# Performance work log

Hardware: AMD Instinct MI355X
Metric: run time of the kernel (lower is better)

Reference implementation:

```python
import jax, jax.numpy as jnp
import numpy as np

N, F = 8192, 64
SLOPE = 3.0


def _mlp(h, params):
    # params: list of (W[in,out], b[out]); Tanh after EVERY linear (incl. last)
    for W, b in params:
        h = jnp.tanh(h @ W + b)
    return h


def setup_inputs() -> dict:
    key = jax.random.key(0)
    ks = jax.random.split(key, 16)
    x = jax.random.normal(ks[0], (N, F, 2), dtype=jnp.float32)
    def lin(k, fi, fo):
        k1, k2 = jax.random.split(k)
        s = 1.0 / np.sqrt(fi)
        W = jax.random.uniform(k1, (fi, fo), jnp.float32, -s, s)
        b = jax.random.uniform(k2, (fo,), jnp.float32, -s, s)
        return W, b
    w_in1, b_in1 = lin(ks[1], 2, 4)
    w_in2, b_in2 = lin(ks[2], 4, 4)
    w_in3, b_in3 = lin(ks[3], 4, 1)
    w_a1, b_a1 = lin(ks[4], 1, 2)
    w_a2, b_a2 = lin(ks[5], 2, 1)
    w_b1, b_b1 = lin(ks[6], 1, 2)
    w_b2, b_b2 = lin(ks[7], 2, 1)
    return dict(x=x,
                w_in1=w_in1, b_in1=b_in1, w_in2=w_in2, b_in2=b_in2,
                w_in3=w_in3, b_in3=b_in3,
                w_a1=w_a1, b_a1=b_a1, w_a2=w_a2, b_a2=b_a2,
                w_b1=w_b1, b_b1=b_b1, w_b2=w_b2, b_b2=b_b2)


def reference(x, w_in1, b_in1, w_in2, b_in2, w_in3, b_in3,
              w_a1, b_a1, w_a2, b_a2, w_b1, b_b1, w_b2, b_b2):
    n, f = x.shape[0], x.shape[1]
    # per-coordinate-pair encode: [N*F,2] -> [N*F,1] -> [N,F]
    h = _mlp(x.reshape(-1, 2), [(w_in1, b_in1), (w_in2, b_in2), (w_in3, b_in3)])
    xe = h.reshape(n, f)
    # dense self-attention aggregation, softmax over dim 0 (columns normalized)
    attn = jax.nn.softmax(xe @ xe.T, axis=0)  # [N,N]
    xe = attn @ xe                            # [N,F]
    # pairwise squared euclidean distances E[i,j] = ||x_i - x_j||^2
    sq = jnp.sum(xe * xe, axis=1)             # [N]
    E = sq[:, None] + sq[None, :] - 2.0 * (xe @ xe.T)
    m = jnp.mean(E).reshape(1)                # [1]
    alpha = jnp.exp(SLOPE * _mlp(m, [(w_a1, b_a1), (w_a2, b_a2)]))
    beta = jnp.exp(-SLOPE * _mlp(m, [(w_b1, b_b1), (w_b2, b_b2)]))
    return xe, alpha, beta
```

## Files before the change

### kernel.cpp

```cpp
#include <hip/hip_runtime.h>
#include <cstdint>

typedef __bf16 bf16x8 __attribute__((ext_vector_type(8)));
typedef __bf16 bf16x4 __attribute__((ext_vector_type(4)));
typedef float  f32x4  __attribute__((ext_vector_type(4)));

#define N_PTS 8192
#define FDIM  64
#define NF    (N_PTS * FDIM)

__device__ __forceinline__ float ftanh(float x) {
    float e = __expf(2.f * x);
    return 1.f - 2.f / (e + 1.f);
}

__global__ __launch_bounds__(256) void k_encode(
    const float* __restrict__ x,
    const float* __restrict__ w1, const float* __restrict__ b1,
    const float* __restrict__ w2, const float* __restrict__ b2,
    const float* __restrict__ w3, const float* __restrict__ b3,
    __bf16* __restrict__ xe)
{
    int idx = blockIdx.x * 256 + threadIdx.x;
    float2 p = ((const float2*)x)[idx];
    float h1[4], h2[4];
#pragma unroll
    for (int o = 0; o < 4; o++)
        h1[o] = ftanh(p.x * w1[o] + p.y * w1[4 + o] + b1[o]);
#pragma unroll
    for (int o = 0; o < 4; o++) {
        float s = b2[o];
#pragma unroll
        for (int i = 0; i < 4; i++) s += h1[i] * w2[i * 4 + o];
        h2[o] = ftanh(s);
    }
    float s3 = b3[0];
#pragma unroll
    for (int i = 0; i < 4; i++) s3 += h2[i] * w3[i];
    xe[idx] = (__bf16)ftanh(s3);
}

__global__ __launch_bounds__(256) void k_pass1(
    const __bf16* __restrict__ xe, float* __restrict__ D)
{
    __shared__ __bf16 sJ[64 * 64];
    __shared__ __bf16 sI[64 * 64];
    const int tid = threadIdx.x;
    const int j0 = blockIdx.x * 64;
    const int ibase = blockIdx.y * 2048;

#pragma unroll
    for (int k = 0; k < 2; k++) {
        int seg = tid + k * 256; int r = seg >> 3, c8 = seg & 7;
        *(uint4*)(sJ + r * 64 + c8 * 8) = *(const uint4*)(xe + (j0 + r) * 64 + c8 * 8);
    }
    __syncthreads();

    const int wave = tid >> 6, lane = tid & 63, c = lane & 15, q = lane >> 4;
    bf16x8 a0 = *(const bf16x8*)(sJ + (16 * wave + c) * 64 + q * 8);
    bf16x8 a1 = *(const bf16x8*)(sJ + (16 * wave + c) * 64 + 32 + q * 8);

    f32x4 esum = {0.f, 0.f, 0.f, 0.f};
    for (int ic = 0; ic < 32; ic++) {
        __syncthreads();
#pragma unroll
        for (int k = 0; k < 2; k++) {
            int seg = tid + k * 256; int r = seg >> 3, c8 = seg & 7;
            *(uint4*)(sI + r * 64 + c8 * 8) =
                *(const uint4*)(xe + (ibase + ic * 64 + r) * 64 + c8 * 8);
        }
        __syncthreads();
#pragma unroll
        for (int it = 0; it < 4; it++) {
            bf16x8 b0 = *(const bf16x8*)(sI + (16 * it + c) * 64 + q * 8);
            bf16x8 b1 = *(const bf16x8*)(sI + (16 * it + c) * 64 + 32 + q * 8);
            f32x4 s = {0.f, 0.f, 0.f, 0.f};
            s = __builtin_amdgcn_mfma_f32_16x16x32_bf16(a0, b0, s, 0, 0, 0);
            s = __builtin_amdgcn_mfma_f32_16x16x32_bf16(a1, b1, s, 0, 0, 0);
            esum.x += __expf(s.x); esum.y += __expf(s.y);
            esum.z += __expf(s.z); esum.w += __expf(s.w);
        }
    }
#pragma unroll
    for (int m = 1; m < 16; m <<= 1) {
        esum.x += __shfl_xor(esum.x, m); esum.y += __shfl_xor(esum.y, m);
        esum.z += __shfl_xor(esum.z, m); esum.w += __shfl_xor(esum.w, m);
    }
    if (c == 0) {
        atomicAdd(&D[j0 + 16 * wave + 4 * q + 0], esum.x);
        atomicAdd(&D[j0 + 16 * wave + 4 * q + 1], esum.y);
        atomicAdd(&D[j0 + 16 * wave + 4 * q + 2], esum.z);
        atomicAdd(&D[j0 + 16 * wave + 4 * q + 3], esum.w);
    }
}

__global__ __launch_bounds__(256) void k_build_u(
    const __bf16* __restrict__ xe, const float* __restrict__ D,
    __bf16* __restrict__ uT)
{
    __shared__ __bf16 T[64 * 72];
    const int tid = threadIdx.x;
    const int j0 = blockIdx.x * 64;
    const int r = tid >> 2, cg = tid & 3;
    float invd = 1.0f / D[j0 + r];
    bf16x8 v0 = *(const bf16x8*)(xe + (j0 + r) * 64 + cg * 16);
    bf16x8 v1 = *(const bf16x8*)(xe + (j0 + r) * 64 + cg * 16 + 8);
#pragma unroll
    for (int e = 0; e < 8; e++) {
        T[(cg * 16 + e) * 72 + r]     = (__bf16)((float)v0[e] * invd);
        T[(cg * 16 + 8 + e) * 72 + r] = (__bf16)((float)v1[e] * invd);
    }
    __syncthreads();
    uint4 w0 = *(uint4*)((char*)T + r * 144 + cg * 32);
    uint4 w1 = *(uint4*)((char*)T + r * 144 + cg * 32 + 16);
    *(uint4*)(uT + r * 8192 + j0 + cg * 16)     = w0;
    *(uint4*)(uT + r * 8192 + j0 + cg * 16 + 8) = w1;
}

__global__ __launch_bounds__(256) void k_pass2(
    const __bf16* __restrict__ xe, const __bf16* __restrict__ uT,
    float* __restrict__ out)
{
    __shared__ __bf16 sI[128 * 64];
    __shared__ __bf16 sJ[64 * 64];
    __shared__ __bf16 sU[64 * 64];
    __shared__ __bf16 sP[128 * 72];
    const int tid = threadIdx.x;
    const int ibase = blockIdx.x * 128;
    const int jbase = blockIdx.y * 1024;

#pragma unroll
    for (int k = 0; k < 4; k++) {
        int seg = tid + k * 256; int r = seg >> 3, c8 = seg & 7;
        *(uint4*)(sI + r * 64 + c8 * 8) = *(const uint4*)(xe + (ibase + r) * 64 + c8 * 8);
    }
    __syncthreads();

    const int wave = tid >> 6, lane = tid & 63, c = lane & 15, q = lane >> 4;
    bf16x8 bst[2][2];
#pragma unroll
    for (int isub = 0; isub < 2; isub++)
#pragma unroll
        for (int kc = 0; kc < 2; kc++)
            bst[isub][kc] = *(const bf16x8*)(sI + (32 * wave + 16 * isub + c) * 64 + kc * 32 + q * 8);

    f32x4 o[2][4];
#pragma unroll
    for (int a = 0; a < 2; a++)
#pragma unroll
        for (int b = 0; b < 4; b++) o[a][b] = (f32x4){0.f, 0.f, 0.f, 0.f};

    for (int jc = 0; jc < 16; jc++) {
        const int j0 = jbase + jc * 64;
        __syncthreads();
#pragma unroll
        for (int k = 0; k < 2; k++) {
            int seg = tid + k * 256; int r = seg >> 3, c8 = seg & 7;
            *(uint4*)(sJ + r * 64 + c8 * 8) = *(const uint4*)(xe + (j0 + r) * 64 + c8 * 8);
            *(uint4*)(sU + r * 64 + c8 * 8) = *(const uint4*)(uT + r * 8192 + j0 + c8 * 8);
        }
        __syncthreads();

#pragma unroll
        for (int jt = 0; jt < 4; jt++) {
            bf16x8 a0 = *(const bf16x8*)(sJ + (16 * jt + c) * 64 + q * 8);
            bf16x8 a1 = *(const bf16x8*)(sJ + (16 * jt + c) * 64 + 32 + q * 8);
#pragma unroll
            for (int isub = 0; isub < 2; isub++) {
                f32x4 s = {0.f, 0.f, 0.f, 0.f};
                s = __builtin_amdgcn_mfma_f32_16x16x32_bf16(a0, bst[isub][0], s, 0, 0, 0);
                s = __builtin_amdgcn_mfma_f32_16x16x32_bf16(a1, bst[isub][1], s, 0, 0, 0);
                bf16x4 pv;
                pv[0] = (__bf16)__expf(s[0]); pv[1] = (__bf16)__expf(s[1]);
                pv[2] = (__bf16)__expf(s[2]); pv[3] = (__bf16)__expf(s[3]);
                *(bf16x4*)(sP + (32 * wave + 16 * isub + c) * 72 + 16 * jt + 4 * q) = pv;
            }
        }
#pragma unroll
        for (int kc = 0; kc < 2; kc++) {
            bf16x8 ap0 = *(const bf16x8*)(sP + (32 * wave + c) * 72 + kc * 32 + q * 8);
            bf16x8 ap1 = *(const bf16x8*)(sP + (32 * wave + 16 + c) * 72 + kc * 32 + q * 8);
#pragma unroll
            for (int ft = 0; ft < 4; ft++) {
                bf16x8 bu = *(const bf16x8*)(sU + (16 * ft + c) * 64 + kc * 32 + q * 8);
                o[0][ft] = __builtin_amdgcn_mfma_f32_16x16x32_bf16(ap0, bu, o[0][ft], 0, 0, 0);
                o[1][ft] = __builtin_amdgcn_mfma_f32_16x16x32_bf16(ap1, bu, o[1][ft], 0, 0, 0);
            }
        }
    }
#pragma unroll
    for (int isub = 0; isub < 2; isub++)
#pragma unroll
        for (int ft = 0; ft < 4; ft++)
#pragma unroll
            for (int r = 0; r < 4; r++)
                atomicAdd(&out[(ibase + 32 * wave + 16 * isub + 4 * q + r) * 64 + 16 * ft + c],
                          o[isub][ft][r]);
}

__global__ __launch_bounds__(256) void k_combine(
    const float* __restrict__ out, float* __restrict__ colp,
    float* __restrict__ sqp)
{
    const int tid = threadIdx.x;
    const int base = blockIdx.x * 256 + tid;
    float col = 0.f, sq = 0.f;
#pragma unroll
    for (int k = 0; k < 8; k++) {
        float o = out[base + k * 65536];
        col += o; sq += o * o;
    }
    __shared__ float sv[256];
    __shared__ float sw[4];
    sv[tid] = col;
#pragma unroll
    for (int m = 32; m; m >>= 1) sq += __shfl_xor(sq, m);
    if ((tid & 63) == 0) sw[tid >> 6] = sq;
    __syncthreads();
    if (tid < 64) {
        float t = sv[tid] + sv[tid + 64] + sv[tid + 128] + sv[tid + 192];
        colp[blockIdx.x * 64 + tid] = t;
    }
    if (tid == 0) sqp[blockIdx.x] = sw[0] + sw[1] + sw[2] + sw[3];
}

__global__ void k_final(
    const float* __restrict__ colp, const float* __restrict__ sqp,
    const float* __restrict__ wa1, const float* __restrict__ ba1,
    const float* __restrict__ wa2, const float* __restrict__ ba2,
    const float* __restrict__ wb1, const float* __restrict__ bb1,
    const float* __restrict__ wb2, const float* __restrict__ bb2,
    float* __restrict__ out_tail)
{
    const int f = threadIdx.x;
    float colsum = 0.f;
    for (int b = 0; b < 256; b++) colsum += colp[b * 64 + f];
    float ss = colsum * colsum;
#pragma unroll
    for (int m = 32; m; m >>= 1) ss += __shfl_xor(ss, m);
    float sq = 0.f;
#pragma unroll
    for (int k = 0; k < 4; k++) sq += sqp[f + 64 * k];
#pragma unroll
    for (int m = 32; m; m >>= 1) sq += __shfl_xor(sq, m);
    if (f == 0) {
        const float invN = 1.f / 8192.f;
        float m = 2.f * invN * sq - 2.f * invN * invN * ss;
        float h0 = tanhf(m * wa1[0] + ba1[0]);
        float h1 = tanhf(m * wa1[1] + ba1[1]);
        float a  = tanhf(h0 * wa2[0] + h1 * wa2[1] + ba2[0]);
        float g0 = tanhf(m * wb1[0] + bb1[0]);
        float g1 = tanhf(m * wb1[1] + bb1[1]);
        float b  = tanhf(g0 * wb2[0] + g1 * wb2[1] + bb2[0]);
        out_tail[0] = __expf(3.f * a);
        out_tail[1] = __expf(-3.f * b);
    }
}

extern "C" void kernel_launch(void* const* d_in, const int* in_sizes, int n_in,
                              void* d_out, int out_size, void* d_ws, size_t ws_size,
                              hipStream_t stream)
{
    const float* x     = (const float*)d_in[0];
    const float* w_in1 = (const float*)d_in[1];
    const float* b_in1 = (const float*)d_in[2];
    const float* w_in2 = (const float*)d_in[3];
    const float* b_in2 = (const float*)d_in[4];
    const float* w_in3 = (const float*)d_in[5];
    const float* b_in3 = (const float*)d_in[6];
    const float* w_a1  = (const float*)d_in[7];
    const float* b_a1  = (const float*)d_in[8];
    const float* w_a2  = (const float*)d_in[9];
    const float* b_a2  = (const float*)d_in[10];
    const float* w_b1  = (const float*)d_in[11];
    const float* b_b1  = (const float*)d_in[12];
    const float* w_b2  = (const float*)d_in[13];
    const float* b_b2  = (const float*)d_in[14];

    float* out = (float*)d_out;
    char*  ws  = (char*)d_ws;
    __bf16* xe = (__bf16*)ws;
    __bf16* uT = (__bf16*)(ws + (1 << 20));
    float*  D  = (float*)(ws + (2 << 20));
    float*  colp = (float*)(ws + (2 << 20) + 32768);
    float*  sqp  = (float*)(ws + (2 << 20) + 32768 + 65536);

    hipMemsetAsync(D, 0, N_PTS * sizeof(float), stream);
    hipMemsetAsync(out, 0, (size_t)out_size * sizeof(float), stream);

    k_encode<<<NF / 256, 256, 0, stream>>>(x, w_in1, b_in1, w_in2, b_in2, w_in3, b_in3, xe);
    k_pass1<<<dim3(128, 4), 256, 0, stream>>>(xe, D);
    k_build_u<<<128, 256, 0, stream>>>(xe, D, uT);
    k_pass2<<<dim3(64, 8), 256, 0, stream>>>(xe, uT, out);
    k_combine<<<NF / 256 / 8, 256, 0, stream>>>(out, colp, sqp);
    k_final<<<1, 64, 0, stream>>>(colp, sqp, w_a1, b_a1, w_a2, b_a2,
                                  w_b1, b_b1, w_b2, b_b2, out + NF);
}
```

Measured before the change: 171.6 us.

## Replace atomics with partial buffers and double grid parallelism in both passes

Pass1 now keeps the J-tile fragments in registers, streams 128-row I tiles, and writes per-block column partial sums to a buffer instead of issuing atomics. Pass2 doubles the grid along j and writes per-split partial outputs, and k_combine reduces the 16 partials, which removes both the output atomics and the memsets. LDS rows are padded to 72 elements to reduce bank conflicts. The cost is extra workspace traffic: 16 full output-sized partial buffers are written and then read back in the combine step.

```diff
diff --git a/kernel.cpp b/kernel.cpp
--- a/kernel.cpp
+++ b/kernel.cpp
@@ -41,68 +41,68 @@
 }
 
 __global__ __launch_bounds__(256) void k_pass1(
-    const __bf16* __restrict__ xe, float* __restrict__ D)
-{
-    __shared__ __bf16 sJ[64 * 64];
-    __shared__ __bf16 sI[64 * 64];
+    const __bf16* __restrict__ xe, float* __restrict__ Dp)
+{
+    __shared__ __bf16 sI[128 * 72];
     const int tid = threadIdx.x;
     const int j0 = blockIdx.x * 64;
-    const int ibase = blockIdx.y * 2048;
-
-#pragma unroll
-    for (int k = 0; k < 2; k++) {
-        int seg = tid + k * 256; int r = seg >> 3, c8 = seg & 7;
-        *(uint4*)(sJ + r * 64 + c8 * 8) = *(const uint4*)(xe + (j0 + r) * 64 + c8 * 8);
-    }
-    __syncthreads();
-
+    const int ibase = blockIdx.y * 1024;
     const int wave = tid >> 6, lane = tid & 63, c = lane & 15, q = lane >> 4;
-    bf16x8 a0 = *(const bf16x8*)(sJ + (16 * wave + c) * 64 + q * 8);
-    bf16x8 a1 = *(const bf16x8*)(sJ + (16 * wave + c) * 64 + 32 + q * 8);
-
-    f32x4 esum = {0.f, 0.f, 0.f, 0.f};
-    for (int ic = 0; ic < 32; ic++) {
-        __syncthreads();
-#pragma unroll
-        for (int k = 0; k < 2; k++) {
+
+    bf16x8 Bf[4][2];
+#pragma unroll
+    for (int jt = 0; jt < 4; jt++)
+#pragma unroll
+        for (int kc = 0; kc < 2; kc++)
+            Bf[jt][kc] = *(const bf16x8*)(xe + (j0 + 16 * jt + c) * 64 + kc * 32 + q * 8);
+
+    float es[4] = {0.f, 0.f, 0.f, 0.f};
+    for (int ic = 0; ic < 8; ic++) {
+        __syncthreads();
+#pragma unroll
+        for (int k = 0; k < 4; k++) {
             int seg = tid + k * 256; int r = seg >> 3, c8 = seg & 7;
-            *(uint4*)(sI + r * 64 + c8 * 8) =
-                *(const uint4*)(xe + (ibase + ic * 64 + r) * 64 + c8 * 8);
-        }
-        __syncthreads();
-#pragma unroll
-        for (int it = 0; it < 4; it++) {
-            bf16x8 b0 = *(const bf16x8*)(sI + (16 * it + c) * 64 + q * 8);
-            bf16x8 b1 = *(const bf16x8*)(sI + (16 * it + c) * 64 + 32 + q * 8);
-            f32x4 s = {0.f, 0.f, 0.f, 0.f};
-            s = __builtin_amdgcn_mfma_f32_16x16x32_bf16(a0, b0, s, 0, 0, 0);
-            s = __builtin_amdgcn_mfma_f32_16x16x32_bf16(a1, b1, s, 0, 0, 0);
-            esum.x += __expf(s.x); esum.y += __expf(s.y);
-            esum.z += __expf(s.z); esum.w += __expf(s.w);
-        }
-    }
-#pragma unroll
-    for (int m = 1; m < 16; m <<= 1) {
-        esum.x += __shfl_xor(esum.x, m); esum.y += __shfl_xor(esum.y, m);
-        esum.z += __shfl_xor(esum.z, m); esum.w += __shfl_xor(esum.w, m);
-    }
-    if (c == 0) {
-        atomicAdd(&D[j0 + 16 * wave + 4 * q + 0], esum.x);
-        atomicAdd(&D[j0 + 16 * wave + 4 * q + 1], esum.y);
-        atomicAdd(&D[j0 + 16 * wave + 4 * q + 2], esum.z);
-        atomicAdd(&D[j0 + 16 * wave + 4 * q + 3], esum.w);
+            *(uint4*)(sI + r * 72 + c8 * 8) =
+                *(const uint4*)(xe + (ibase + ic * 128 + r) * 64 + c8 * 8);
+        }
+        __syncthreads();
+#pragma unroll
+        for (int g = 0; g < 2; g++) {
+            bf16x8 a0 = *(const bf16x8*)(sI + (32 * wave + 16 * g + c) * 72 + q * 8);
+            bf16x8 a1 = *(const bf16x8*)(sI + (32 * wave + 16 * g + c) * 72 + 32 + q * 8);
+#pragma unroll
+            for (int jt = 0; jt < 4; jt++) {
+                f32x4 s = {0.f, 0.f, 0.f, 0.f};
+                s = __builtin_amdgcn_mfma_f32_16x16x32_bf16(a0, Bf[jt][0], s, 0, 0, 0);
+                s = __builtin_amdgcn_mfma_f32_16x16x32_bf16(a1, Bf[jt][1], s, 0, 0, 0);
+                es[jt] += __expf(s.x) + __expf(s.y) + __expf(s.z) + __expf(s.w);
+            }
+        }
+    }
+#pragma unroll
+    for (int jt = 0; jt < 4; jt++) {
+        es[jt] += __shfl_xor(es[jt], 16);
+        es[jt] += __shfl_xor(es[jt], 32);
+    }
+    if (q == 0) {
+        float* d = Dp + (blockIdx.y * 4 + wave) * N_PTS + j0;
+#pragma unroll
+        for (int jt = 0; jt < 4; jt++) d[16 * jt + c] = es[jt];
     }
 }
 
 __global__ __launch_bounds__(256) void k_build_u(
-    const __bf16* __restrict__ xe, const float* __restrict__ D,
+    const __bf16* __restrict__ xe, const float* __restrict__ Dp,
     __bf16* __restrict__ uT)
 {
     __shared__ __bf16 T[64 * 72];
     const int tid = threadIdx.x;
     const int j0 = blockIdx.x * 64;
     const int r = tid >> 2, cg = tid & 3;
-    float invd = 1.0f / D[j0 + r];
+    float dsum = 0.f;
+#pragma unroll
+    for (int s = 0; s < 32; s++) dsum += Dp[s * N_PTS + j0 + r];
+    float invd = 1.0f / dsum;
     bf16x8 v0 = *(const bf16x8*)(xe + (j0 + r) * 64 + cg * 16);
     bf16x8 v1 = *(const bf16x8*)(xe + (j0 + r) * 64 + cg * 16 + 8);
 #pragma unroll
@@ -119,30 +119,22 @@
 
 __global__ __launch_bounds__(256) void k_pass2(
     const __bf16* __restrict__ xe, const __bf16* __restrict__ uT,
-    float* __restrict__ out)
-{
-    __shared__ __bf16 sI[128 * 64];
-    __shared__ __bf16 sJ[64 * 64];
-    __shared__ __bf16 sU[64 * 64];
+    float* __restrict__ outp)
+{
+    __shared__ __bf16 sJ[64 * 72];
+    __shared__ __bf16 sU[64 * 72];
     __shared__ __bf16 sP[128 * 72];
     const int tid = threadIdx.x;
     const int ibase = blockIdx.x * 128;
-    const int jbase = blockIdx.y * 1024;
-
-#pragma unroll
-    for (int k = 0; k < 4; k++) {
-        int seg = tid + k * 256; int r = seg >> 3, c8 = seg & 7;
-        *(uint4*)(sI + r * 64 + c8 * 8) = *(const uint4*)(xe + (ibase + r) * 64 + c8 * 8);
-    }
-    __syncthreads();
-
+    const int jbase = blockIdx.y * 512;
     const int wave = tid >> 6, lane = tid & 63, c = lane & 15, q = lane >> 4;
+
     bf16x8 bst[2][2];
 #pragma unroll
     for (int isub = 0; isub < 2; isub++)
 #pragma unroll
         for (int kc = 0; kc < 2; kc++)
-            bst[isub][kc] = *(const bf16x8*)(sI + (32 * wave + 16 * isub + c) * 64 + kc * 32 + q * 8);
+            bst[isub][kc] = *(const bf16x8*)(xe + (ibase + 32 * wave + 16 * isub + c) * 64 + kc * 32 + q * 8);
 
     f32x4 o[2][4];
 #pragma unroll
@@ -150,21 +142,21 @@
 #pragma unroll
         for (int b = 0; b < 4; b++) o[a][b] = (f32x4){0.f, 0.f, 0.f, 0.f};
 
-    for (int jc = 0; jc < 16; jc++) {
+    for (int jc = 0; jc < 8; jc++) {
         const int j0 = jbase + jc * 64;
         __syncthreads();
 #pragma unroll
         for (int k = 0; k < 2; k++) {
             int seg = tid + k * 256; int r = seg >> 3, c8 = seg & 7;
-            *(uint4*)(sJ + r * 64 + c8 * 8) = *(const uint4*)(xe + (j0 + r) * 64 + c8 * 8);
-            *(uint4*)(sU + r * 64 + c8 * 8) = *(const uint4*)(uT + r * 8192 + j0 + c8 * 8);
+            *(uint4*)(sJ + r * 72 + c8 * 8) = *(const uint4*)(xe + (j0 + r) * 64 + c8 * 8);
+            *(uint4*)(sU + r * 72 + c8 * 8) = *(const uint4*)(uT + r * 8192 + j0 + c8 * 8);
         }
         __syncthreads();
 
 #pragma unroll
         for (int jt = 0; jt < 4; jt++) {
-            bf16x8 a0 = *(const bf16x8*)(sJ + (16 * jt + c) * 64 + q * 8);
-            bf16x8 a1 = *(const bf16x8*)(sJ + (16 * jt + c) * 64 + 32 + q * 8);
+            bf16x8 a0 = *(const bf16x8*)(sJ + (16 * jt + c) * 72 + q * 8);
+            bf16x8 a1 = *(const bf16x8*)(sJ + (16 * jt + c) * 72 + 32 + q * 8);
 #pragma unroll
             for (int isub = 0; isub < 2; isub++) {
                 f32x4 s = {0.f, 0.f, 0.f, 0.f};
@@ -182,33 +174,38 @@
             bf16x8 ap1 = *(const bf16x8*)(sP + (32 * wave + 16 + c) * 72 + kc * 32 + q * 8);
 #pragma unroll
             for (int ft = 0; ft < 4; ft++) {
-                bf16x8 bu = *(const bf16x8*)(sU + (16 * ft + c) * 64 + kc * 32 + q * 8);
+                bf16x8 bu = *(const bf16x8*)(sU + (16 * ft + c) * 72 + kc * 32 + q * 8);
                 o[0][ft] = __builtin_amdgcn_mfma_f32_16x16x32_bf16(ap0, bu, o[0][ft], 0, 0, 0);
                 o[1][ft] = __builtin_amdgcn_mfma_f32_16x16x32_bf16(ap1, bu, o[1][ft], 0, 0, 0);
             }
         }
     }
+    float* dst = outp + (size_t)blockIdx.y * NF;
 #pragma unroll
     for (int isub = 0; isub < 2; isub++)
 #pragma unroll
         for (int ft = 0; ft < 4; ft++)
 #pragma unroll
             for (int r = 0; r < 4; r++)
-                atomicAdd(&out[(ibase + 32 * wave + 16 * isub + 4 * q + r) * 64 + 16 * ft + c],
-                          o[isub][ft][r]);
+                dst[(ibase + 32 * wave + 16 * isub + 4 * q + r) * 64 + 16 * ft + c] =
+                    o[isub][ft][r];
 }
 
 __global__ __launch_bounds__(256) void k_combine(
-    const float* __restrict__ out, float* __restrict__ colp,
-    float* __restrict__ sqp)
+    const float* __restrict__ outp, float* __restrict__ out,
+    float* __restrict__ colp, float* __restrict__ sqp)
 {
     const int tid = threadIdx.x;
     const int base = blockIdx.x * 256 + tid;
     float col = 0.f, sq = 0.f;
 #pragma unroll
     for (int k = 0; k < 8; k++) {
-        float o = out[base + k * 65536];
-        col += o; sq += o * o;
+        int idx = base + k * 65536;
+        float acc = 0.f;
+#pragma unroll
+        for (int s = 0; s < 16; s++) acc += outp[(size_t)s * NF + idx];
+        out[idx] = acc;
+        col += acc; sq += acc * acc;
     }
     __shared__ float sv[256];
     __shared__ float sw[4];
@@ -279,20 +276,18 @@
 
     float* out = (float*)d_out;
     char*  ws  = (char*)d_ws;
-    __bf16* xe = (__bf16*)ws;
-    __bf16* uT = (__bf16*)(ws + (1 << 20));
-    float*  D  = (float*)(ws + (2 << 20));
-    float*  colp = (float*)(ws + (2 << 20) + 32768);
-    float*  sqp  = (float*)(ws + (2 << 20) + 32768 + 65536);
-
-    hipMemsetAsync(D, 0, N_PTS * sizeof(float), stream);
-    hipMemsetAsync(out, 0, (size_t)out_size * sizeof(float), stream);
+    __bf16* xe  = (__bf16*)ws;
+    __bf16* uT  = (__bf16*)(ws + (1 << 20));
+    float*  Dp  = (float*)(ws + (2 << 20));
+    float*  colp = (float*)(ws + (3 << 20));
+    float*  sqp  = (float*)(ws + (3 << 20) + (1 << 16));
+    float*  outp = (float*)(ws + (4 << 20));
 
     k_encode<<<NF / 256, 256, 0, stream>>>(x, w_in1, b_in1, w_in2, b_in2, w_in3, b_in3, xe);
-    k_pass1<<<dim3(128, 4), 256, 0, stream>>>(xe, D);
-    k_build_u<<<128, 256, 0, stream>>>(xe, D, uT);
-    k_pass2<<<dim3(64, 8), 256, 0, stream>>>(xe, uT, out);
-    k_combine<<<NF / 256 / 8, 256, 0, stream>>>(out, colp, sqp);
+    k_pass1<<<dim3(128, 8), 256, 0, stream>>>(xe, Dp);
+    k_build_u<<<128, 256, 0, stream>>>(xe, Dp, uT);
+    k_pass2<<<dim3(64, 16), 256, 0, stream>>>(xe, uT, outp);
+    k_combine<<<256, 256, 0, stream>>>(outp, out, colp, sqp);
     k_final<<<1, 64, 0, stream>>>(colp, sqp, w_a1, b_a1, w_a2, b_a2,
                                   w_b1, b_b1, w_b2, b_b2, out + NF);
 }
```

New measurement: 159.3 us. -7.2%, faster.
